# Kernel tuning notes

Hardware: AMD Instinct MI355X
Metric: run time of the kernel (lower is better)

The kernel has to match this reference:

```python
import jax, jax.numpy as jnp
import numpy as np

N = 50000        # nodes
E = 250000       # edges (avg degree 5)
D = 32           # embed_dim
N_LAYERS = 3


def _uniform(key, shape, fan_in):
    s = 1.0 / np.sqrt(fan_in)
    return jax.random.uniform(key, shape, jnp.float32, -s, s)


def setup_inputs() -> dict:
    key = jax.random.key(0)
    ks = jax.random.split(key, 10)
    x = jax.random.normal(ks[0], (N, 1), jnp.float32)
    edge_index = jax.random.randint(ks[1], (2, E), 0, N, dtype=jnp.int64)
    edge_attribute = jax.random.normal(ks[2], (E, 1), jnp.float32)
    # Linear weights stored as [in, out] (i.e. torch weight transposed)
    node_W = _uniform(ks[3], (1, D), 1)
    node_b = _uniform(ks[4], (D,), 1)
    l1_W = _uniform(ks[5], (1, D * D), 1)
    l1_b = _uniform(ks[6], (D * D,), 1)
    root = _uniform(ks[7], (D, D), D)      # NNConv root weight
    conv_b = _uniform(ks[8], (D,), D)      # NNConv bias
    return {
        "x": x, "edge_index": edge_index, "edge_attribute": edge_attribute,
        "i": 2, "dummy": 0,
        "node_W": node_W, "node_b": node_b,
        "l1_W": l1_W, "l1_b": l1_b,
        "root": root, "conv_b": conv_b,
    }


def reference(x, edge_index, edge_attribute, i, dummy, node_W, node_b,
              l1_W, l1_b, root, conv_b):
    n_encode_layers = min(i + 1, N_LAYERS)
    src, dst = edge_index[0], edge_index[1]

    # node embedding: [N,1] -> [N,D]
    h = x @ node_W + node_b

    # edge-conditioned weight matrices, shared by every layer: [E, D, D]
    We = (edge_attribute @ l1_W + l1_b).reshape(E, D, D)

    # mean-aggregation denominator (in-degree, clamped; isolated nodes -> 0 msg)
    cnt = jax.ops.segment_sum(jnp.ones((E,), h.dtype), dst, num_segments=N)
    cnt = jnp.maximum(cnt, 1.0)[:, None]

    for _ in range(n_encode_layers):
        h = jax.nn.relu(h)
        # gather source features, per-edge matmul: msg_e = x_src[e] @ We[e]
        msg = jnp.einsum('ei,eio->eo', h[src], We)
        aggr = jax.ops.segment_sum(msg, dst, num_segments=N) / cnt
        h = aggr + h @ root + conv_b
    return h
```

## Files before the change

### kernel.cpp

```cpp
#include <hip/hip_runtime.h>
#include <hip/hip_bf16.h>

#define N_NODES 50000
#define N_EDGES 250000
#define DIM 32
#define BLK 256
#define CAP 16
#define SPILL_MAX 4096
#define EDGE_NB 977
#define WCONV_NB 13
#define LAYER_NB 3125
#define POISON 0xAAAAAAAAu

typedef __attribute__((ext_vector_type(8))) short short8;
typedef __attribute__((ext_vector_type(4))) float f32x4;

__device__ __forceinline__ float ldf(const void* p, int i, int isf32) {
    return isf32 ? ((const float*)p)[i]
                 : __bfloat162float(((const __hip_bfloat16*)p)[i]);
}
__device__ __forceinline__ float b2f(unsigned int u16) {
    return __uint_as_float(u16 << 16);
}
__device__ __forceinline__ int ldi(const int* ei, int i, int i64) {
    return i64 ? ei[2 * i] : ei[i];
}
__device__ __forceinline__ int clamp_idx(int v) {
    v = v < 0 ? 0 : v;
    return v >= N_NODES ? N_NODES - 1 : v;
}
__device__ __forceinline__ bool half_is_big(const void* p, int k) {
    unsigned short h = ((const unsigned short*)p)[k];
    float v = __uint_as_float(((unsigned int)h) << 16);
    return !(fabsf(v) <= 50.0f);
}
__device__ __forceinline__ unsigned short bf16bits(float v) {
    __hip_bfloat16 b = __float2bfloat16(v);
    return __builtin_bit_cast(unsigned short, b);
}
__device__ __forceinline__ unsigned int pack2(float lo, float hi) {
    return ((unsigned int)bf16bits(hi) << 16) | (unsigned int)bf16bits(lo);
}

__global__ __launch_bounds__(BLK) void prep_kernel(
    const int* __restrict__ ei, const void* __restrict__ ea,
    const void* __restrict__ lW, const void* __restrict__ lb,
    const void* __restrict__ rt, const void* __restrict__ cb,
    int* __restrict__ cntI, int2* __restrict__ packed,
    int* __restrict__ spill_cnt, int4* __restrict__ spill,
    float* __restrict__ wCB, unsigned short* __restrict__ wfrag)
{
    __shared__ int sdet;
    int tid = threadIdx.x;
    int b = blockIdx.x;
    if (tid == 0) sdet = 0;
    __syncthreads();

    if (b < EDGE_NB) {
        if (tid < 64) {
            if (ei[2 * tid + 1] != 0) atomicOr(&sdet, 2);
        } else if (tid < 192) {
            if (half_is_big(ea, tid - 64)) atomicOr(&sdet, 1);
        }
        __syncthreads();
        int f_ea = sdet & 1, i64 = ((sdet & 2) == 0);
        int e = b * BLK + tid;
        if (e < N_EDGES) {
            int s = clamp_idx(ldi(ei, e, i64));
            int d = clamp_idx(ldi(ei, N_EDGES + e, i64));
            float a = ldf(ea, e, f_ea);
            unsigned k = (unsigned)atomicAdd(&cntI[d], 1) - POISON;
            if (k < CAP) {
                packed[d * CAP + (int)k] = make_int2(s, __float_as_int(a));
            } else {
                unsigned sp = (unsigned)atomicAdd(spill_cnt, 1) - POISON;
                if (sp < SPILL_MAX)
                    spill[sp] = make_int4(d, s, __float_as_int(a), 0);
            }
        }
        return;
    }

    if (tid < 64)       { if (half_is_big(lW, tid) || half_is_big(lW, tid + 64)) atomicOr(&sdet, 1); }
    else if (tid < 128) { int k = tid - 64;  if (half_is_big(lb, k) || half_is_big(lb, k + 64)) atomicOr(&sdet, 2); }
    else if (tid < 192) { int k = tid - 128; if (half_is_big(rt, k) || half_is_big(rt, k + 64)) atomicOr(&sdet, 4); }
    else if (tid < 224) { if (half_is_big(cb, tid - 192)) atomicOr(&sdet, 8); }
    __syncthreads();
    int fW = sdet & 1, fB = sdet & 2, fR = sdet & 4, fC = sdet & 8;
    int g = (int)(b - EDGE_NB) * BLK + tid;
    if (g < 3072) {
        int f = g >> 9, rem = g & 511;
        int ln = rem >> 3, j = rem & 7;
        int t = f >> 1, nh = f & 1;
        int k = t * 32 + (ln >> 4) * 8 + j;
        int n = nh * 16 + (ln & 15);
        float v;
        if (k < 32)      v = ldf(lW, k * 32 + n, fW);
        else if (k < 64) v = ldf(lb, (k - 32) * 32 + n, fB);
        else             v = ldf(rt, (k - 64) * 32 + n, fR);
        wfrag[g] = bf16bits(v);
    } else if (g < 3104) {
        wCB[g - 3072] = ldf(cb, g - 3072, fC);
    }
}

__global__ __launch_bounds__(256) void layer_kernel(
    const int2* __restrict__ packed, const int* __restrict__ cntI,
    const int* __restrict__ spill_cnt, const int4* __restrict__ spill,
    const void* __restrict__ x, const void* __restrict__ nW,
    const void* __restrict__ nb,
    const unsigned int* __restrict__ hin,
    const float* __restrict__ wCB,
    const unsigned short* __restrict__ wfrag,
    void* __restrict__ outb, int mode0, int last)
{
    __shared__ __align__(16) unsigned int sAu32[16 * 48];
    __shared__ int sdet;
    int tid = threadIdx.x;
    int wv = tid >> 6;
    int lane = tid & 63;
    int q = lane >> 4;
    int l16 = lane & 15;
    int nbase = blockIdx.x * 16;
    int n0 = nbase + wv * 4;

    float nW2lo = 0.0f, nW2hi = 0.0f, nb2lo = 0.0f, nb2hi = 0.0f;
    int f_x = 0;
    if (mode0) {
        if (tid == 0) sdet = 0;
        __syncthreads();
        if (tid < 128) {
            if (half_is_big(x, tid)) atomicOr(&sdet, 4);
        } else if (tid < 160) {
            if (half_is_big(nW, tid - 128)) atomicOr(&sdet, 8);
        } else if (tid < 192) {
            if (half_is_big(nb, tid - 160)) atomicOr(&sdet, 16);
        }
        __syncthreads();
        f_x = sdet & 4;
        nW2lo = ldf(nW, 2 * l16,     sdet & 8);
        nW2hi = ldf(nW, 2 * l16 + 1, sdet & 8);
        nb2lo = ldf(nb, 2 * l16,     sdet & 16);
        nb2hi = ldf(nb, 2 * l16 + 1, sdet & 16);
    }

    int4 c[4];
    #pragma unroll
    for (int j = 0; j < 4; ++j)
        c[j] = *(const int4*)(packed + (n0 + j) * CAP + 2 * q);

    int deg[4];
    {
        int4 d4 = *(const int4*)(cntI + n0);
        deg[0] = (int)((unsigned)d4.x - POISON);
        deg[1] = (int)((unsigned)d4.y - POISON);
        deg[2] = (int)((unsigned)d4.z - POISON);
        deg[3] = (int)((unsigned)d4.w - POISON);
    }

    float hslo, hshi;
    {
        int ns = clamp_idx(n0 + q);
        if (mode0) {
            float xs = ldf(x, ns, f_x);
            hslo = fmaf(xs, nW2lo, nb2lo); hslo = hslo > 0.0f ? hslo : 0.0f;
            hshi = fmaf(xs, nW2hi, nb2hi); hshi = hshi > 0.0f ? hshi : 0.0f;
        } else {
            unsigned int u = hin[ns * 16 + l16];
            hslo = b2f(u & 0xffffu);
            hshi = b2f(u >> 16);
        }
    }

    float plo[4] = {0,0,0,0}, phi[4] = {0,0,0,0};
    float qlo[4] = {0,0,0,0}, qhi[4] = {0,0,0,0};
    #pragma unroll
    for (int j = 0; j < 4; ++j) {
        int s0 = clamp_idx(c[j].x), s1 = clamp_idx(c[j].z);
        float a0 = __int_as_float(c[j].y), a1 = __int_as_float(c[j].w);
        float h0lo, h0hi, h1lo, h1hi;
        if (mode0) {
            float xs0 = ldf(x, s0, f_x), xs1 = ldf(x, s1, f_x);
            h0lo = fmaf(xs0, nW2lo, nb2lo); h0lo = h0lo > 0.0f ? h0lo : 0.0f;
            h0hi = fmaf(xs0, nW2hi, nb2hi); h0hi = h0hi > 0.0f ? h0hi : 0.0f;
            h1lo = fmaf(xs1, nW2lo, nb2lo); h1lo = h1lo > 0.0f ? h1lo : 0.0f;
            h1hi = fmaf(xs1, nW2hi, nb2hi); h1hi = h1hi > 0.0f ? h1hi : 0.0f;
        } else {
            unsigned int u0 = hin[s0 * 16 + l16];
            unsigned int u1 = hin[s1 * 16 + l16];
            h0lo = b2f(u0 & 0xffffu); h0hi = b2f(u0 >> 16);
            h1lo = b2f(u1 & 0xffffu); h1hi = b2f(u1 >> 16);
        }
        bool v0 = (2 * q)     < deg[j];
        bool v1 = (2 * q + 1) < deg[j];
        float a0m = v0 ? a0 : 0.0f, a1m = v1 ? a1 : 0.0f;
        float h0lom = v0 ? h0lo : 0.0f, h0him = v0 ? h0hi : 0.0f;
        float h1lom = v1 ? h1lo : 0.0f, h1him = v1 ? h1hi : 0.0f;
        plo[j] = fmaf(a0m, h0lom, plo[j]); plo[j] = fmaf(a1m, h1lom, plo[j]);
        phi[j] = fmaf(a0m, h0him, phi[j]); phi[j] = fmaf(a1m, h1him, phi[j]);
        qlo[j] += h0lom + h1lom;
        qhi[j] += h0him + h1him;
    }
    #pragma unroll
    for (int j = 0; j < 4; ++j) {
        if (deg[j] > 8) {
            int4 c2 = *(const int4*)(packed + (n0 + j) * CAP + 8 + 2 * q);
            int dgc = deg[j] < CAP ? deg[j] : CAP;
            int s0 = clamp_idx(c2.x), s1 = clamp_idx(c2.z);
            float a0 = __int_as_float(c2.y), a1 = __int_as_float(c2.w);
            float h0lo, h0hi, h1lo, h1hi;
            if (mode0) {
                float xs0 = ldf(x, s0, f_x), xs1 = ldf(x, s1, f_x);
                h0lo = fmaf(xs0, nW2lo, nb2lo); h0lo = h0lo > 0.0f ? h0lo : 0.0f;
                h0hi = fmaf(xs0, nW2hi, nb2hi); h0hi = h0hi > 0.0f ? h0hi : 0.0f;
                h1lo = fmaf(xs1, nW2lo, nb2lo); h1lo = h1lo > 0.0f ? h1lo : 0.0f;
                h1hi = fmaf(xs1, nW2hi, nb2hi); h1hi = h1hi > 0.0f ? h1hi : 0.0f;
            } else {
                unsigned int u0 = hin[s0 * 16 + l16];
                unsigned int u1 = hin[s1 * 16 + l16];
                h0lo = b2f(u0 & 0xffffu); h0hi = b2f(u0 >> 16);
                h1lo = b2f(u1 & 0xffffu); h1hi = b2f(u1 >> 16);
            }
            bool v0 = (8 + 2 * q)     < dgc;
            bool v1 = (8 + 2 * q + 1) < dgc;
            float a0m = v0 ? a0 : 0.0f, a1m = v1 ? a1 : 0.0f;
            float h0lom = v0 ? h0lo : 0.0f, h0him = v0 ? h0hi : 0.0f;
            float h1lom = v1 ? h1lo : 0.0f, h1him = v1 ? h1hi : 0.0f;
            plo[j] = fmaf(a0m, h0lom, plo[j]); plo[j] = fmaf(a1m, h1lom, plo[j]);
            phi[j] = fmaf(a0m, h0him, phi[j]); phi[j] = fmaf(a1m, h1him, phi[j]);
            qlo[j] += h0lom + h1lom;
            qhi[j] += h0him + h1him;
        }
    }
    unsigned spt = (unsigned)(*spill_cnt) - POISON;
    if (spt != 0) {
        if (spt > SPILL_MAX) spt = SPILL_MAX;
        #pragma unroll
        for (int j = 0; j < 4; ++j) {
            if (deg[j] > CAP) {
                for (unsigned t = (unsigned)q; t < spt; t += 4) {
                    int4 sp = spill[t];
                    if (sp.x == n0 + j) {
                        float hvlo, hvhi;
                        if (mode0) {
                            float xs = ldf(x, clamp_idx(sp.y), f_x);
                            hvlo = fmaf(xs, nW2lo, nb2lo); hvlo = hvlo > 0.0f ? hvlo : 0.0f;
                            hvhi = fmaf(xs, nW2hi, nb2hi); hvhi = hvhi > 0.0f ? hvhi : 0.0f;
                        } else {
                            unsigned int u = hin[clamp_idx(sp.y) * 16 + l16];
                            hvlo = b2f(u & 0xffffu); hvhi = b2f(u >> 16);
                        }
                        float a = __int_as_float(sp.z);
                        plo[j] = fmaf(a, hvlo, plo[j]);
                        phi[j] = fmaf(a, hvhi, phi[j]);
                        qlo[j] += hvlo; qhi[j] += hvhi;
                    }
                }
            }
        }
    }
    #pragma unroll
    for (int j = 0; j < 4; ++j) {
        plo[j] += __shfl_xor(plo[j], 16); plo[j] += __shfl_xor(plo[j], 32);
        phi[j] += __shfl_xor(phi[j], 16); phi[j] += __shfl_xor(phi[j], 32);
        qlo[j] += __shfl_xor(qlo[j], 16); qlo[j] += __shfl_xor(qlo[j], 32);
        qhi[j] += __shfl_xor(qhi[j], 16); qhi[j] += __shfl_xor(qhi[j], 32);
    }
    #pragma unroll
    for (int j = 0; j < 4; ++j) {
        float ic = 1.0f / (deg[j] < 1 ? 1.0f : (float)deg[j]);
        if (q == 0)
            sAu32[(wv * 4 + j) * 48 + l16]      = pack2(plo[j] * ic, phi[j] * ic);
        else if (q == 1)
            sAu32[(wv * 4 + j) * 48 + 16 + l16] = pack2(qlo[j] * ic, qhi[j] * ic);
    }
    sAu32[(wv * 4 + q) * 48 + 32 + l16] = pack2(hslo, hshi);
    __syncthreads();

    if (wv < 2) {
        const unsigned short* sAu = (const unsigned short*)sAu32;
        int nh = wv;
        short8 bfr[3];
        #pragma unroll
        for (int t = 0; t < 3; ++t)
            bfr[t] = *(const short8*)(wfrag + ((t * 2 + nh) * 64 + lane) * 8);
        f32x4 acc = {0.0f, 0.0f, 0.0f, 0.0f};
        #pragma unroll
        for (int t = 0; t < 3; ++t) {
            short8 afr = *(const short8*)(sAu + (lane & 15) * 96
                                          + t * 32 + (lane >> 4) * 8);
            acc = __builtin_amdgcn_mfma_f32_16x16x32_bf16(afr, bfr[t], acc, 0, 0, 0);
        }
        float cbl = wCB[nh * 16 + (lane & 15)];
        #pragma unroll
        for (int r = 0; r < 4; ++r) {
            int row = (lane >> 4) * 4 + r;
            int n = nbase + row;
            if (n < N_NODES) {
                float v = acc[r] + cbl;
                int col = nh * 16 + (lane & 15);
                if (!last) {
                    v = v > 0.0f ? v : 0.0f;
                    ((unsigned short*)outb)[n * DIM + col] = bf16bits(v);
                } else {
                    ((float*)outb)[n * DIM + col] = v;
                }
            }
        }
    }
}

extern "C" void kernel_launch(void* const* d_in, const int* in_sizes, int n_in,
                              void* d_out, int out_size, void* d_ws, size_t ws_size,
                              hipStream_t stream) {
    const void* p[16];
    int np_ = 0;
    for (int i = 0; i < n_in && np_ < 16; ++i)
        if (in_sizes[i] != 1) p[np_++] = d_in[i];

    const void* x      = p[0];
    const int*  ei     = (const int*)p[1];
    const void* ea     = p[2];
    const void* node_W = p[3];
    const void* node_b = p[4];
    const void* l1_W   = p[5];
    const void* l1_b   = p[6];
    const void* root   = p[7];
    const void* conv_b = p[8];
    float* out = (float*)d_out;

    char* ws = (char*)d_ws;
    int2*  packed    = (int2*)ws;
    unsigned int* hr1 = (unsigned int*)(packed + N_NODES * CAP);
    unsigned int* hr2 = hr1 + N_NODES * 16;
    float* wCB       = (float*)(hr2 + N_NODES * 16);
    unsigned short* wfrag = (unsigned short*)(wCB + 32);
    int*   cntI      = (int*)(wfrag + 3072);
    int*   spill_cnt = cntI + N_NODES;
    int4*  spill     = (int4*)(spill_cnt + 4);

    prep_kernel<<<EDGE_NB + WCONV_NB, BLK, 0, stream>>>(
        ei, ea, l1_W, l1_b, root, conv_b,
        cntI, packed, spill_cnt, spill, wCB, wfrag);

    layer_kernel<<<LAYER_NB, 256, 0, stream>>>(packed, cntI, spill_cnt, spill,
        x, node_W, node_b, hr2 , wCB, wfrag, hr1, 1, 0);
    layer_kernel<<<LAYER_NB, 256, 0, stream>>>(packed, cntI, spill_cnt, spill,
        x, node_W, node_b, hr1, wCB, wfrag, hr2, 0, 0);
    layer_kernel<<<LAYER_NB, 256, 0, stream>>>(packed, cntI, spill_cnt, spill,
        x, node_W, node_b, hr2, wCB, wfrag, out, 0, 1);
}
```

Before: 133.2 us.

## Make each wavefront own a full 16-node tile and drop block-wide barrier

Each wavefront now processes 16 nodes in four sequential groups of four, writing into its own private LDS tile, then runs both MFMA column halves itself. This removes the block-level __syncthreads and the idle waves in the MFMA phase, and quarters the grid size. In exchange the gather loop is serialized per wave (unroll 1), so there is less memory-level parallelism per wave and fewer blocks in flight, which may expose gather latency.

```diff
diff --git a/kernel.cpp b/kernel.cpp
--- a/kernel.cpp
+++ b/kernel.cpp
@@ -9,7 +9,7 @@
 #define SPILL_MAX 4096
 #define EDGE_NB 977
 #define WCONV_NB 13
-#define LAYER_NB 3125
+#define LAYER_NB 782
 #define POISON 0xAAAAAAAAu
 
 typedef __attribute__((ext_vector_type(8))) short short8;
@@ -114,15 +114,14 @@
     const unsigned short* __restrict__ wfrag,
     void* __restrict__ outb, int mode0, int last)
 {
-    __shared__ __align__(16) unsigned int sAu32[16 * 48];
+    __shared__ __align__(16) unsigned int sAu32[4][16 * 48];
     __shared__ int sdet;
     int tid = threadIdx.x;
     int wv = tid >> 6;
     int lane = tid & 63;
     int q = lane >> 4;
     int l16 = lane & 15;
-    int nbase = blockIdx.x * 16;
-    int n0 = nbase + wv * 4;
+    int wn0 = (blockIdx.x * 4 + wv) * 16;
 
     float nW2lo = 0.0f, nW2hi = 0.0f, nb2lo = 0.0f, nb2hi = 0.0f;
     int f_x = 0;
@@ -144,70 +143,54 @@
         nb2hi = ldf(nb, 2 * l16 + 1, sdet & 16);
     }
 
-    int4 c[4];
-    #pragma unroll
-    for (int j = 0; j < 4; ++j)
-        c[j] = *(const int4*)(packed + (n0 + j) * CAP + 2 * q);
-
-    int deg[4];
-    {
-        int4 d4 = *(const int4*)(cntI + n0);
-        deg[0] = (int)((unsigned)d4.x - POISON);
-        deg[1] = (int)((unsigned)d4.y - POISON);
-        deg[2] = (int)((unsigned)d4.z - POISON);
-        deg[3] = (int)((unsigned)d4.w - POISON);
-    }
-
-    float hslo, hshi;
-    {
-        int ns = clamp_idx(n0 + q);
-        if (mode0) {
-            float xs = ldf(x, ns, f_x);
-            hslo = fmaf(xs, nW2lo, nb2lo); hslo = hslo > 0.0f ? hslo : 0.0f;
-            hshi = fmaf(xs, nW2hi, nb2hi); hshi = hshi > 0.0f ? hshi : 0.0f;
+    unsigned spt = (unsigned)(*spill_cnt) - POISON;
+    if (spt > SPILL_MAX) spt = SPILL_MAX;
+    unsigned int* sw = sAu32[wv];
+
+    #pragma unroll 1
+    for (int g = 0; g < 4; ++g) {
+        int n0 = wn0 + g * 4;
+
+        int4 c[4];
+        #pragma unroll
+        for (int j = 0; j < 4; ++j)
+            c[j] = *(const int4*)(packed + clamp_idx(n0 + j) * CAP + 2 * q);
+
+        int deg[4];
+        if (n0 + 3 < N_NODES) {
+            int4 d4 = *(const int4*)(cntI + n0);
+            deg[0] = (int)((unsigned)d4.x - POISON);
+            deg[1] = (int)((unsigned)d4.y - POISON);
+            deg[2] = (int)((unsigned)d4.z - POISON);
+            deg[3] = (int)((unsigned)d4.w - POISON);
         } else {
-            unsigned int u = hin[ns * 16 + l16];
-            hslo = b2f(u & 0xffffu);
-            hshi = b2f(u >> 16);
-        }
-    }
-
-    float plo[4] = {0,0,0,0}, phi[4] = {0,0,0,0};
-    float qlo[4] = {0,0,0,0}, qhi[4] = {0,0,0,0};
-    #pragma unroll
-    for (int j = 0; j < 4; ++j) {
-        int s0 = clamp_idx(c[j].x), s1 = clamp_idx(c[j].z);
-        float a0 = __int_as_float(c[j].y), a1 = __int_as_float(c[j].w);
-        float h0lo, h0hi, h1lo, h1hi;
-        if (mode0) {
-            float xs0 = ldf(x, s0, f_x), xs1 = ldf(x, s1, f_x);
-            h0lo = fmaf(xs0, nW2lo, nb2lo); h0lo = h0lo > 0.0f ? h0lo : 0.0f;
-            h0hi = fmaf(xs0, nW2hi, nb2hi); h0hi = h0hi > 0.0f ? h0hi : 0.0f;
-            h1lo = fmaf(xs1, nW2lo, nb2lo); h1lo = h1lo > 0.0f ? h1lo : 0.0f;
-            h1hi = fmaf(xs1, nW2hi, nb2hi); h1hi = h1hi > 0.0f ? h1hi : 0.0f;
-        } else {
-            unsigned int u0 = hin[s0 * 16 + l16];
-            unsigned int u1 = hin[s1 * 16 + l16];
-            h0lo = b2f(u0 & 0xffffu); h0hi = b2f(u0 >> 16);
-            h1lo = b2f(u1 & 0xffffu); h1hi = b2f(u1 >> 16);
-        }
-        bool v0 = (2 * q)     < deg[j];
-        bool v1 = (2 * q + 1) < deg[j];
-        float a0m = v0 ? a0 : 0.0f, a1m = v1 ? a1 : 0.0f;
-        float h0lom = v0 ? h0lo : 0.0f, h0him = v0 ? h0hi : 0.0f;
-        float h1lom = v1 ? h1lo : 0.0f, h1him = v1 ? h1hi : 0.0f;
-        plo[j] = fmaf(a0m, h0lom, plo[j]); plo[j] = fmaf(a1m, h1lom, plo[j]);
-        phi[j] = fmaf(a0m, h0him, phi[j]); phi[j] = fmaf(a1m, h1him, phi[j]);
-        qlo[j] += h0lom + h1lom;
-        qhi[j] += h0him + h1him;
-    }
-    #pragma unroll
-    for (int j = 0; j < 4; ++j) {
-        if (deg[j] > 8) {
-            int4 c2 = *(const int4*)(packed + (n0 + j) * CAP + 8 + 2 * q);
-            int dgc = deg[j] < CAP ? deg[j] : CAP;
-            int s0 = clamp_idx(c2.x), s1 = clamp_idx(c2.z);
-            float a0 = __int_as_float(c2.y), a1 = __int_as_float(c2.w);
+            #pragma unroll
+            for (int j = 0; j < 4; ++j) {
+                int n = n0 + j;
+                deg[j] = (n < N_NODES) ? (int)((unsigned)cntI[n] - POISON) : 0;
+            }
+        }
+
+        float hslo, hshi;
+        {
+            int ns = clamp_idx(n0 + q);
+            if (mode0) {
+                float xs = ldf(x, ns, f_x);
+                hslo = fmaf(xs, nW2lo, nb2lo); hslo = hslo > 0.0f ? hslo : 0.0f;
+                hshi = fmaf(xs, nW2hi, nb2hi); hshi = hshi > 0.0f ? hshi : 0.0f;
+            } else {
+                unsigned int u = hin[ns * 16 + l16];
+                hslo = b2f(u & 0xffffu);
+                hshi = b2f(u >> 16);
+            }
+        }
+
+        float plo[4] = {0,0,0,0}, phi[4] = {0,0,0,0};
+        float qlo[4] = {0,0,0,0}, qhi[4] = {0,0,0,0};
+        #pragma unroll
+        for (int j = 0; j < 4; ++j) {
+            int s0 = clamp_idx(c[j].x), s1 = clamp_idx(c[j].z);
+            float a0 = __int_as_float(c[j].y), a1 = __int_as_float(c[j].w);
             float h0lo, h0hi, h1lo, h1hi;
             if (mode0) {
                 float xs0 = ldf(x, s0, f_x), xs1 = ldf(x, s1, f_x);
@@ -221,8 +204,8 @@
                 h0lo = b2f(u0 & 0xffffu); h0hi = b2f(u0 >> 16);
                 h1lo = b2f(u1 & 0xffffu); h1hi = b2f(u1 >> 16);
             }
-            bool v0 = (8 + 2 * q)     < dgc;
-            bool v1 = (8 + 2 * q + 1) < dgc;
+            bool v0 = (2 * q)     < deg[j];
+            bool v1 = (2 * q + 1) < deg[j];
             float a0m = v0 ? a0 : 0.0f, a1m = v1 ? a1 : 0.0f;
             float h0lom = v0 ? h0lo : 0.0f, h0him = v0 ? h0hi : 0.0f;
             float h1lom = v1 ? h1lo : 0.0f, h1him = v1 ? h1hi : 0.0f;
@@ -231,55 +214,83 @@
             qlo[j] += h0lom + h1lom;
             qhi[j] += h0him + h1him;
         }
-    }
-    unsigned spt = (unsigned)(*spill_cnt) - POISON;
-    if (spt != 0) {
-        if (spt > SPILL_MAX) spt = SPILL_MAX;
         #pragma unroll
         for (int j = 0; j < 4; ++j) {
-            if (deg[j] > CAP) {
-                for (unsigned t = (unsigned)q; t < spt; t += 4) {
-                    int4 sp = spill[t];
-                    if (sp.x == n0 + j) {
-                        float hvlo, hvhi;
-                        if (mode0) {
-                            float xs = ldf(x, clamp_idx(sp.y), f_x);
-                            hvlo = fmaf(xs, nW2lo, nb2lo); hvlo = hvlo > 0.0f ? hvlo : 0.0f;
-                            hvhi = fmaf(xs, nW2hi, nb2hi); hvhi = hvhi > 0.0f ? hvhi : 0.0f;
-                        } else {
-                            unsigned int u = hin[clamp_idx(sp.y) * 16 + l16];
-                            hvlo = b2f(u & 0xffffu); hvhi = b2f(u >> 16);
+            if (deg[j] > 8) {
+                int4 c2 = *(const int4*)(packed + clamp_idx(n0 + j) * CAP + 8 + 2 * q);
+                int dgc = deg[j] < CAP ? deg[j] : CAP;
+                int s0 = clamp_idx(c2.x), s1 = clamp_idx(c2.z);
+                float a0 = __int_as_float(c2.y), a1 = __int_as_float(c2.w);
+                float h0lo, h0hi, h1lo, h1hi;
+                if (mode0) {
+                    float xs0 = ldf(x, s0, f_x), xs1 = ldf(x, s1, f_x);
+                    h0lo = fmaf(xs0, nW2lo, nb2lo); h0lo = h0lo > 0.0f ? h0lo : 0.0f;
+                    h0hi = fmaf(xs0, nW2hi, nb2hi); h0hi = h0hi > 0.0f ? h0hi : 0.0f;
+                    h1lo = fmaf(xs1, nW2lo, nb2lo); h1lo = h1lo > 0.0f ? h1lo : 0.0f;
+                    h1hi = fmaf(xs1, nW2hi, nb2hi); h1hi = h1hi > 0.0f ? h1hi : 0.0f;
+                } else {
+                    unsigned int u0 = hin[s0 * 16 + l16];
+                    unsigned int u1 = hin[s1 * 16 + l16];
+                    h0lo = b2f(u0 & 0xffffu); h0hi = b2f(u0 >> 16);
+                    h1lo = b2f(u1 & 0xffffu); h1hi = b2f(u1 >> 16);
+                }
+                bool v0 = (8 + 2 * q)     < dgc;
+                bool v1 = (8 + 2 * q + 1) < dgc;
+                float a0m = v0 ? a0 : 0.0f, a1m = v1 ? a1 : 0.0f;
+                float h0lom = v0 ? h0lo : 0.0f, h0him = v0 ? h0hi : 0.0f;
+                float h1lom = v1 ? h1lo : 0.0f, h1him = v1 ? h1hi : 0.0f;
+                plo[j] = fmaf(a0m, h0lom, plo[j]); plo[j] = fmaf(a1m, h1lom, plo[j]);
+                phi[j] = fmaf(a0m, h0him, phi[j]); phi[j] = fmaf(a1m, h1him, phi[j]);
+                qlo[j] += h0lom + h1lom;
+                qhi[j] += h0him + h1him;
+            }
+        }
+        if (spt != 0) {
+            #pragma unroll
+            for (int j = 0; j < 4; ++j) {
+                if (deg[j] > CAP) {
+                    for (unsigned t = (unsigned)q; t < spt; t += 4) {
+                        int4 sp = spill[t];
+                        if (sp.x == n0 + j) {
+                            float hvlo, hvhi;
+                            if (mode0) {
+                                float xs = ldf(x, clamp_idx(sp.y), f_x);
+                                hvlo = fmaf(xs, nW2lo, nb2lo); hvlo = hvlo > 0.0f ? hvlo : 0.0f;
+                                hvhi = fmaf(xs, nW2hi, nb2hi); hvhi = hvhi > 0.0f ? hvhi : 0.0f;
+                            } else {
+                                unsigned int u = hin[clamp_idx(sp.y) * 16 + l16];
+                                hvlo = b2f(u & 0xffffu); hvhi = b2f(u >> 16);
+                            }
+                            float a = __int_as_float(sp.z);
+                            plo[j] = fmaf(a, hvlo, plo[j]);
+                            phi[j] = fmaf(a, hvhi, phi[j]);
+                            qlo[j] += hvlo; qhi[j] += hvhi;
                         }
-                        float a = __int_as_float(sp.z);
-                        plo[j] = fmaf(a, hvlo, plo[j]);
-                        phi[j] = fmaf(a, hvhi, phi[j]);
-                        qlo[j] += hvlo; qhi[j] += hvhi;
                     }
                 }
             }
         }
-    }
+        #pragma unroll
+        for (int j = 0; j < 4; ++j) {
+            plo[j] += __shfl_xor(plo[j], 16); plo[j] += __shfl_xor(plo[j], 32);
+            phi[j] += __shfl_xor(phi[j], 16); phi[j] += __shfl_xor(phi[j], 32);
+            qlo[j] += __shfl_xor(qlo[j], 16); qlo[j] += __shfl_xor(qlo[j], 32);
+            qhi[j] += __shfl_xor(qhi[j], 16); qhi[j] += __shfl_xor(qhi[j], 32);
+        }
+        #pragma unroll
+        for (int j = 0; j < 4; ++j) {
+            float ic = 1.0f / (deg[j] < 1 ? 1.0f : (float)deg[j]);
+            if (q == 0)
+                sw[(g * 4 + j) * 48 + l16]      = pack2(plo[j] * ic, phi[j] * ic);
+            else if (q == 1)
+                sw[(g * 4 + j) * 48 + 16 + l16] = pack2(qlo[j] * ic, qhi[j] * ic);
+        }
+        sw[(g * 4 + q) * 48 + 32 + l16] = pack2(hslo, hshi);
+    }
+
+    const unsigned short* sAu = (const unsigned short*)sw;
     #pragma unroll
-    for (int j = 0; j < 4; ++j) {
-        plo[j] += __shfl_xor(plo[j], 16); plo[j] += __shfl_xor(plo[j], 32);
-        phi[j] += __shfl_xor(phi[j], 16); phi[j] += __shfl_xor(phi[j], 32);
-        qlo[j] += __shfl_xor(qlo[j], 16); qlo[j] += __shfl_xor(qlo[j], 32);
-        qhi[j] += __shfl_xor(qhi[j], 16); qhi[j] += __shfl_xor(qhi[j], 32);
-    }
-    #pragma unroll
-    for (int j = 0; j < 4; ++j) {
-        float ic = 1.0f / (deg[j] < 1 ? 1.0f : (float)deg[j]);
-        if (q == 0)
-            sAu32[(wv * 4 + j) * 48 + l16]      = pack2(plo[j] * ic, phi[j] * ic);
-        else if (q == 1)
-            sAu32[(wv * 4 + j) * 48 + 16 + l16] = pack2(qlo[j] * ic, qhi[j] * ic);
-    }
-    sAu32[(wv * 4 + q) * 48 + 32 + l16] = pack2(hslo, hshi);
-    __syncthreads();
-
-    if (wv < 2) {
-        const unsigned short* sAu = (const unsigned short*)sAu32;
-        int nh = wv;
+    for (int nh = 0; nh < 2; ++nh) {
         short8 bfr[3];
         #pragma unroll
         for (int t = 0; t < 3; ++t)
@@ -295,7 +306,7 @@
         #pragma unroll
         for (int r = 0; r < 4; ++r) {
             int row = (lane >> 4) * 4 + r;
-            int n = nbase + row;
+            int n = wn0 + row;
             if (n < N_NODES) {
                 float v = acc[r] + cbl;
                 int col = nh * 16 + (lane & 15);
```

New measurement: 147.8 us. +11.0%, slower.
